# Kernel tuning notes

Hardware: AMD Instinct MI355X
Metric: run time of the kernel (lower is better)

The kernel has to match this reference:

```python
import jax, jax.numpy as jnp
import numpy as np

D_MODEL = 1024
NUM_HEADS = 16
D_HEAD = D_MODEL // NUM_HEADS
PATCH = 128


def setup_inputs() -> dict:
    key = jax.random.key(0)
    ks = jax.random.split(key, 10)
    B, T = 4, 8192
    x = jax.random.normal(ks[0], (B, T, D_MODEL), dtype=jnp.float32)
    coords = jax.random.uniform(ks[1], (B, T, 2), dtype=jnp.float32)
    s = 1.0 / np.sqrt(D_MODEL)
    Wq = jax.random.normal(ks[2], (D_MODEL, D_MODEL), dtype=jnp.float32) * s
    Wk = jax.random.normal(ks[3], (D_MODEL, D_MODEL), dtype=jnp.float32) * s
    Wv = jax.random.normal(ks[4], (D_MODEL, D_MODEL), dtype=jnp.float32) * s
    Wo = jax.random.normal(ks[5], (D_MODEL, D_MODEL), dtype=jnp.float32) * s
    bq = jnp.zeros((D_MODEL,), jnp.float32)
    bk = jnp.zeros((D_MODEL,), jnp.float32)
    bv = jnp.zeros((D_MODEL,), jnp.float32)
    bo = jnp.zeros((D_MODEL,), jnp.float32)
    return {"x": x, "coords": coords, "Wq": Wq, "bq": bq, "Wk": Wk, "bk": bk,
            "Wv": Wv, "bv": bv, "Wo": Wo, "bo": bo}


def _patched_attn(x, Wq, bq, Wk, bk, Wv, bv, Wo, bo):
    B, T, D = x.shape
    P = PATCH
    pad_len = (P - T % P) % P
    if pad_len > 0:
        x = jnp.pad(x, ((0, 0), (0, pad_len), (0, 0)))
    Tp = T + pad_len
    n = Tp // P
    xp = x.reshape(B * n, P, D)  # [N, P, D], independent patches
    def heads(y):  # [N, P, D] -> [N, H, P, dh]
        return y.reshape(B * n, P, NUM_HEADS, D_HEAD).transpose(0, 2, 1, 3)
    q = heads(xp @ Wq + bq)
    k = heads(xp @ Wk + bk)
    v = heads(xp @ Wv + bv)
    scores = jnp.einsum('bhtd,bhTd->bhtT', q, k) / jnp.sqrt(jnp.asarray(D_HEAD, x.dtype))
    w = jax.nn.softmax(scores, axis=-1)
    out = jnp.einsum('bhtT,bhTd->bhtd', w, v)
    out = out.transpose(0, 2, 1, 3).reshape(B * n, P, D)
    out = out @ Wo + bo
    out = out.reshape(B, Tp, D)
    if pad_len > 0:
        out = out[:, :T, :]
    return out


def reference(x, coords, Wq, bq, Wk, bk, Wv, bv, Wo, bo):
    # coords participates only in padding/reshape, not in the math
    return _patched_attn(x, Wq, bq, Wk, bk, Wv, bv, Wo, bo)
```

## Files before the change

### kernel.cpp

```cpp
#include <hip/hip_runtime.h>
#include <hip/hip_bf16.h>


#define DEV static __device__ __forceinline__

typedef __attribute__((ext_vector_type(8))) short short8;
typedef __attribute__((ext_vector_type(4))) float f32x4;

DEV unsigned short f2b(float f) {
  unsigned u = __builtin_bit_cast(unsigned, f);
  u += 0x7fffu + ((u >> 16) & 1u);
  return (unsigned short)(u >> 16);
}

DEV void load_lds16(const void* g, void* l) {
  __builtin_amdgcn_global_load_lds(
      (const __attribute__((address_space(1))) void*)g,
      (__attribute__((address_space(3))) void*)l, 16, 0, 0);
}

#define MFMA_BF16(a, b, c) __builtin_amdgcn_mfma_f32_16x16x32_bf16((a), (b), (c), 0, 0, 0)


__global__ void cvt_x_k(const float* __restrict__ x, unsigned short* __restrict__ xb, int n4) {
  int i = blockIdx.x * blockDim.x + threadIdx.x;
  int stride = gridDim.x * blockDim.x;
  for (; i < n4; i += stride) {
    float4 v = ((const float4*)x)[i];
    ushort4 o;
    o.x = f2b(v.x); o.y = f2b(v.y); o.z = f2b(v.z); o.w = f2b(v.w);
    ((ushort4*)xb)[i] = o;
  }
}

__global__ void twk4(const float* __restrict__ W0, const float* __restrict__ W1,
                     const float* __restrict__ W2, const float* __restrict__ W3,
                     unsigned short* __restrict__ Dqkv, unsigned short* __restrict__ Dot) {
  __shared__ unsigned short tile[64][65];
  const int w = blockIdx.x >> 8;
  const int t = blockIdx.x & 255;
  const float* W = (w == 0) ? W0 : (w == 1) ? W1 : (w == 2) ? W2 : W3;
  unsigned short* Wt = (w == 3) ? Dot : Dqkv + (size_t)w * 1024 * 1024;
  int k0 = (t >> 4) << 6;
  int n0 = (t & 15) << 6;
  int tx = threadIdx.x & 63;
  int ty = threadIdx.x >> 6;
#pragma unroll
  for (int i = 0; i < 16; ++i) {
    int r = (i << 2) + ty;
    tile[r][tx] = f2b(W[(size_t)(k0 + r) * 1024 + n0 + tx]);
  }
  __syncthreads();
#pragma unroll
  for (int i = 0; i < 16; ++i) {
    int n = (i << 2) + ty;
    Wt[(size_t)(n0 + n) * 1024 + k0 + tx] = tile[tx][n];
  }
}

__global__ void fuse_bias_k(const float* __restrict__ bq, const float* __restrict__ bk,
                            const float* __restrict__ bv, float* __restrict__ bqkv) {
  int i = blockIdx.x * 256 + threadIdx.x;
  if (i < 1024) bqkv[i] = bq[i];
  else if (i < 2048) bqkv[i] = bk[i - 1024];
  else if (i < 3072) bqkv[i] = bv[i - 2048];
}


template <bool OUT_F32>
__global__ __launch_bounds__(512, 2)
void gemm256(const unsigned short* __restrict__ A,
             const unsigned short* __restrict__ Bt,
             const float* __restrict__ bias,
             void* __restrict__ Cv, int M, int N, int K) {
  __shared__ __align__(16) unsigned short sh[65536];

  int nwg = gridDim.x, bid = blockIdx.x, wg = bid;
  if ((nwg & 7) == 0) {
    int cpx = nwg >> 3;
    wg = (bid & 7) * cpx + (bid >> 3);
  }
  const int nbn = N >> 8;
  const int bm = wg / nbn, bn = wg - bm * nbn;

  const int tid = threadIdx.x, lane = tid & 63, w = tid >> 6;
  const int wm = w >> 2, wn = w & 3;
  const int fr = lane & 15, g = lane >> 4;

  const int lr = lane >> 3;
  const int lb = ((lane & 7) << 4) ^ (lr << 4);
  const unsigned short* gsrc = (w < 4)
      ? A  + (size_t)(bm * 256 + w * 64 + lr) * K + (lb >> 1)
      : Bt + (size_t)(bn * 256 + (w - 4) * 64 + lr) * K + (lb >> 1);
  const int ldsw = w * 8192;

  const int koff0 = (g * 16) ^ ((fr & 7) << 4);
  const int koff1 = koff0 ^ 64;

  f32x4 acc[8][4] = {};
  const int NT = K >> 6;

  {
    char* l0 = (char*)sh + ldsw;
#pragma unroll
    for (int c = 0; c < 8; ++c)
      load_lds16(gsrc + (size_t)c * 8 * K, l0 + c * 1024);
  }

  for (int t = 0; t < NT; ++t) {
    if (t + 1 < NT) {
      const unsigned short* sN = gsrc + (size_t)(t + 1) * 64;
      char* lN = (char*)sh + ((t + 1) & 1) * 65536 + ldsw;
#pragma unroll
      for (int c = 0; c < 8; ++c)
        load_lds16(sN + (size_t)c * 8 * K, lN + c * 1024);
      asm volatile("s_waitcnt vmcnt(8)" ::: "memory");
    } else {
      asm volatile("s_waitcnt vmcnt(0)" ::: "memory");
    }
    __builtin_amdgcn_sched_barrier(0);
    __builtin_amdgcn_s_barrier();

    const char* bufp = (const char*)sh + (t & 1) * 65536;
    const char* ap0 = bufp + (wm * 128 + fr) * 128;
    const char* bp0 = bufp + 32768 + (wn * 64 + fr) * 128;

#pragma unroll
    for (int q = 0; q < 4; ++q) {
      const int mh = q >> 1, nh = q & 1;
      short8 af[4][2], bf[2][2];
      const char* ap = ap0 + mh * 64 * 128;
      const char* bp = bp0 + nh * 32 * 128;
#pragma unroll
      for (int ii = 0; ii < 4; ++ii) {
        af[ii][0] = *(const short8*)(ap + ii * 2048 + koff0);
        af[ii][1] = *(const short8*)(ap + ii * 2048 + koff1);
      }
#pragma unroll
      for (int jj = 0; jj < 2; ++jj) {
        bf[jj][0] = *(const short8*)(bp + jj * 2048 + koff0);
        bf[jj][1] = *(const short8*)(bp + jj * 2048 + koff1);
      }
      __builtin_amdgcn_s_barrier();
      asm volatile("s_waitcnt lgkmcnt(0)" ::: "memory");
      __builtin_amdgcn_sched_barrier(0);
      __builtin_amdgcn_s_setprio(1);
#pragma unroll
      for (int s = 0; s < 2; ++s)
#pragma unroll
        for (int ii = 0; ii < 4; ++ii)
#pragma unroll
          for (int jj = 0; jj < 2; ++jj)
            acc[mh * 4 + ii][nh * 2 + jj] =
                MFMA_BF16(af[ii][s], bf[jj][s], acc[mh * 4 + ii][nh * 2 + jj]);
      __builtin_amdgcn_s_setprio(0);
      __builtin_amdgcn_s_barrier();
    }
  }

  const int grow0 = bm * 256 + wm * 128 + g * 4;
  const int gcol0 = bn * 256 + wn * 64 + fr;
#pragma unroll
  for (int j = 0; j < 4; ++j) {
    const int gc = gcol0 + j * 16;
    const float bv_ = bias[gc];
#pragma unroll
    for (int i = 0; i < 8; ++i) {
      const int gr = grow0 + i * 16;
#pragma unroll
      for (int r = 0; r < 4; ++r) {
        float v = acc[i][j][r] + bv_;
        if (OUT_F32) ((float*)Cv)[(size_t)(gr + r) * N + gc] = v;
        else ((unsigned short*)Cv)[(size_t)(gr + r) * N + gc] = f2b(v);
      }
    }
  }
}


__global__ __launch_bounds__(256)
void attn_k(const unsigned short* __restrict__ qkv, unsigned short* __restrict__ out) {
  const int bh = blockIdx.x;
  const int p = bh >> 4, h = bh & 15;
  const int tid = threadIdx.x, lane = tid & 63, wv = tid >> 6;
  const int fr = lane & 15, fks = (lane >> 4) << 3;

  __shared__ __align__(16) unsigned short vt[64][136];
  __shared__ __align__(16) unsigned short pls[4][32][136];

  const size_t rowbase = (size_t)p * 128 * 3072;

  {
    const unsigned short* vsrc = qkv + rowbase + 2048 + (size_t)h * 64;
#pragma unroll
    for (int it = 0; it < 8; ++it) {
      int idx = tid + it * 256;
      int t = idx >> 4;
      int d4 = (idx & 15) << 2;
      ushort4 vv = *(const ushort4*)(vsrc + (size_t)t * 3072 + d4);
      vt[d4 + 0][t] = vv.x; vt[d4 + 1][t] = vv.y;
      vt[d4 + 2][t] = vv.z; vt[d4 + 3][t] = vv.w;
    }
  }

  short8 qf[2][2];
  {
    const unsigned short* qsrc = qkv + rowbase + (size_t)(wv * 32) * 3072 + h * 64;
#pragma unroll
    for (int mf = 0; mf < 2; ++mf)
#pragma unroll
      for (int kc = 0; kc < 2; ++kc)
        qf[mf][kc] = *(const short8*)(qsrc + (size_t)(mf * 16 + fr) * 3072 + kc * 32 + fks);
  }

  f32x4 s[2][8] = {};
  {
    const unsigned short* ksrc = qkv + rowbase + 1024 + (size_t)h * 64;
#pragma unroll
    for (int kc = 0; kc < 2; ++kc)
#pragma unroll
      for (int nf = 0; nf < 8; ++nf) {
        short8 kf = *(const short8*)(ksrc + (size_t)(nf * 16 + fr) * 3072 + kc * 32 + fks);
        s[0][nf] = MFMA_BF16(qf[0][kc], kf, s[0][nf]);
        s[1][nf] = MFMA_BF16(qf[1][kc], kf, s[1][nf]);
      }
  }
  __syncthreads();

  const float c0 = 0.125f * 1.44269504088896f;
  float sm[2][4];
#pragma unroll
  for (int mf = 0; mf < 2; ++mf)
#pragma unroll
    for (int r = 0; r < 4; ++r) {
      float m = s[mf][0][r];
#pragma unroll
      for (int nf = 1; nf < 8; ++nf) m = fmaxf(m, s[mf][nf][r]);
      m = fmaxf(m, __shfl_xor(m, 1));
      m = fmaxf(m, __shfl_xor(m, 2));
      m = fmaxf(m, __shfl_xor(m, 4));
      m = fmaxf(m, __shfl_xor(m, 8));
      float su = 0.f;
#pragma unroll
      for (int nf = 0; nf < 8; ++nf) {
        float e = exp2f((s[mf][nf][r] - m) * c0);
        s[mf][nf][r] = e;
        su += e;
      }
      su += __shfl_xor(su, 1);
      su += __shfl_xor(su, 2);
      su += __shfl_xor(su, 4);
      su += __shfl_xor(su, 8);
      sm[mf][r] = su;
    }

#pragma unroll
  for (int mf = 0; mf < 2; ++mf)
#pragma unroll
    for (int nf = 0; nf < 8; ++nf)
#pragma unroll
      for (int r = 0; r < 4; ++r)
        pls[wv][mf * 16 + ((lane >> 4) << 2) + r][nf * 16 + fr] = f2b(s[mf][nf][r]);

  f32x4 o[2][4] = {};
#pragma unroll
  for (int kc = 0; kc < 4; ++kc) {
    short8 pf0 = *(const short8*)&pls[wv][fr][kc * 32 + fks];
    short8 pf1 = *(const short8*)&pls[wv][16 + fr][kc * 32 + fks];
#pragma unroll
    for (int nf = 0; nf < 4; ++nf) {
      short8 vf = *(const short8*)&vt[nf * 16 + fr][kc * 32 + fks];
      o[0][nf] = MFMA_BF16(pf0, vf, o[0][nf]);
      o[1][nf] = MFMA_BF16(pf1, vf, o[1][nf]);
    }
  }

  unsigned short* obase = out + (size_t)(p * 128 + wv * 32) * 1024 + h * 64;
#pragma unroll
  for (int mf = 0; mf < 2; ++mf)
#pragma unroll
    for (int nf = 0; nf < 4; ++nf)
#pragma unroll
      for (int r = 0; r < 4; ++r) {
        int row = mf * 16 + ((lane >> 4) << 2) + r;
        float val = o[mf][nf][r] / sm[mf][r];
        obase[(size_t)row * 1024 + nf * 16 + fr] = f2b(val);
      }
}


extern "C" void kernel_launch(void* const* d_in, const int* in_sizes, int n_in,
                              void* d_out, int out_size, void* d_ws, size_t ws_size,
                              hipStream_t stream) {
  const float* x  = (const float*)d_in[0];
  const float* Wq = (const float*)d_in[2];
  const float* bq = (const float*)d_in[3];
  const float* Wk = (const float*)d_in[4];
  const float* bk = (const float*)d_in[5];
  const float* Wv = (const float*)d_in[6];
  const float* bv = (const float*)d_in[7];
  const float* Wo = (const float*)d_in[8];
  const float* bo = (const float*)d_in[9];

  char* ws = (char*)d_ws;
  unsigned short* xb   = (unsigned short*)(ws);
  unsigned short* wqkv = (unsigned short*)(ws + 67108864);
  unsigned short* wot  = (unsigned short*)(ws + 73400320);
  float*          bqkv = (float*)(ws + 75497472);
  unsigned short* qkv  = (unsigned short*)(ws + 75509760);

  cvt_x_k<<<2048, 256, 0, stream>>>(x, xb, (32768 * 1024) / 4);
  twk4<<<1024, 256, 0, stream>>>(Wq, Wk, Wv, Wo, wqkv, wot);
  fuse_bias_k<<<12, 256, 0, stream>>>(bq, bk, bv, bqkv);

  gemm256<false><<<1536, 512, 0, stream>>>(xb, wqkv, bqkv, qkv, 32768, 3072, 1024);
  attn_k<<<4096, 256, 0, stream>>>(qkv, xb);
  gemm256<true><<<512, 512, 0, stream>>>(xb, wot, bo, d_out, 32768, 1024, 1024);
}
```

Baseline: 718.7 us.

## Software-pipeline LDS fragment loads across GEMM quadrants with register double buffering

Restructures the GEMM main loop so LDS fragment reads for the next quadrant, and for the next K-tile, are issued while the MFMAs of the current quadrant run. It uses separate a0/a1/b0/b1 register sets and reorders the quadrants so A and B fragments get reused. This is meant to hide LDS latency that the old code exposed before each quadrant by waiting on lgkmcnt(0). The cost is higher register pressure and more complicated barrier and waitcnt logic, which could lower occupancy or add stalls. The epilogue loop order is also changed so that the bias loads are hoisted.

```diff
diff --git a/kernel.cpp b/kernel.cpp
--- a/kernel.cpp
+++ b/kernel.cpp
@@ -20,6 +20,8 @@
 }
 
 #define MFMA_BF16(a, b, c) __builtin_amdgcn_mfma_f32_16x16x32_bf16((a), (b), (c), 0, 0, 0)
+#define SB0() __builtin_amdgcn_sched_barrier(0)
+#define BAR() __builtin_amdgcn_s_barrier()
 
 
 __global__ void cvt_x_k(const float* __restrict__ x, unsigned short* __restrict__ xb, int n4) {
@@ -100,78 +102,138 @@
   f32x4 acc[8][4] = {};
   const int NT = K >> 6;
 
+  short8 a0[4][2], a1[4][2], b0[2][2], b1[2][2];
+
   {
     char* l0 = (char*)sh + ldsw;
 #pragma unroll
     for (int c = 0; c < 8; ++c)
       load_lds16(gsrc + (size_t)c * 8 * K, l0 + c * 1024);
+    asm volatile("s_waitcnt vmcnt(0)" ::: "memory");
+    BAR();
+    const char* ap = (const char*)sh + (wm * 128 + fr) * 128;
+    const char* bp = (const char*)sh + 32768 + (wn * 64 + fr) * 128;
+#pragma unroll
+    for (int ii = 0; ii < 4; ++ii) {
+      a0[ii][0] = *(const short8*)(ap + ii * 2048 + koff0);
+      a0[ii][1] = *(const short8*)(ap + ii * 2048 + koff1);
+    }
+#pragma unroll
+    for (int jj = 0; jj < 2; ++jj) {
+      b0[jj][0] = *(const short8*)(bp + jj * 2048 + koff0);
+      b0[jj][1] = *(const short8*)(bp + jj * 2048 + koff1);
+    }
   }
 
   for (int t = 0; t < NT; ++t) {
+    const char* bufc = (const char*)sh + (t & 1) * 65536;
+    const char* bufn = (const char*)sh + ((t + 1) & 1) * 65536;
+    const char* apc = bufc + (wm * 128 + fr) * 128;
+    const char* bpc = bufc + 32768 + (wn * 64 + fr) * 128;
+
     if (t + 1 < NT) {
       const unsigned short* sN = gsrc + (size_t)(t + 1) * 64;
       char* lN = (char*)sh + ((t + 1) & 1) * 65536 + ldsw;
 #pragma unroll
       for (int c = 0; c < 8; ++c)
         load_lds16(sN + (size_t)c * 8 * K, lN + c * 1024);
-      asm volatile("s_waitcnt vmcnt(8)" ::: "memory");
-    } else {
-      asm volatile("s_waitcnt vmcnt(0)" ::: "memory");
-    }
-    __builtin_amdgcn_sched_barrier(0);
-    __builtin_amdgcn_s_barrier();
-
-    const char* bufp = (const char*)sh + (t & 1) * 65536;
-    const char* ap0 = bufp + (wm * 128 + fr) * 128;
-    const char* bp0 = bufp + 32768 + (wn * 64 + fr) * 128;
-
-#pragma unroll
-    for (int q = 0; q < 4; ++q) {
-      const int mh = q >> 1, nh = q & 1;
-      short8 af[4][2], bf[2][2];
-      const char* ap = ap0 + mh * 64 * 128;
-      const char* bp = bp0 + nh * 32 * 128;
+    }
+#pragma unroll
+    for (int jj = 0; jj < 2; ++jj) {
+      b1[jj][0] = *(const short8*)(bpc + 32 * 128 + jj * 2048 + koff0);
+      b1[jj][1] = *(const short8*)(bpc + 32 * 128 + jj * 2048 + koff1);
+    }
+    BAR();
+    asm volatile("s_waitcnt lgkmcnt(4)" ::: "memory");
+    SB0();
+    __builtin_amdgcn_s_setprio(1);
+#pragma unroll
+    for (int s = 0; s < 2; ++s)
+#pragma unroll
+      for (int ii = 0; ii < 4; ++ii)
+#pragma unroll
+        for (int jj = 0; jj < 2; ++jj)
+          acc[ii][jj] = MFMA_BF16(a0[ii][s], b0[jj][s], acc[ii][jj]);
+    __builtin_amdgcn_s_setprio(0);
+    BAR();
+
+#pragma unroll
+    for (int ii = 0; ii < 4; ++ii) {
+      a1[ii][0] = *(const short8*)(apc + 64 * 128 + ii * 2048 + koff0);
+      a1[ii][1] = *(const short8*)(apc + 64 * 128 + ii * 2048 + koff1);
+    }
+    BAR();
+    asm volatile("s_waitcnt lgkmcnt(8)" ::: "memory");
+    SB0();
+    __builtin_amdgcn_s_setprio(1);
+#pragma unroll
+    for (int s = 0; s < 2; ++s)
+#pragma unroll
+      for (int ii = 0; ii < 4; ++ii)
+#pragma unroll
+        for (int jj = 0; jj < 2; ++jj)
+          acc[ii][2 + jj] = MFMA_BF16(a0[ii][s], b1[jj][s], acc[ii][2 + jj]);
+    __builtin_amdgcn_s_setprio(0);
+    BAR();
+
+    asm volatile("s_waitcnt vmcnt(0)" ::: "memory");
+    BAR();
+    asm volatile("s_waitcnt lgkmcnt(0)" ::: "memory");
+    SB0();
+    __builtin_amdgcn_s_setprio(1);
+#pragma unroll
+    for (int s = 0; s < 2; ++s)
+#pragma unroll
+      for (int ii = 0; ii < 4; ++ii)
+#pragma unroll
+        for (int jj = 0; jj < 2; ++jj)
+          acc[4 + ii][2 + jj] = MFMA_BF16(a1[ii][s], b1[jj][s], acc[4 + ii][2 + jj]);
+    __builtin_amdgcn_s_setprio(0);
+    BAR();
+
+    __builtin_amdgcn_s_setprio(1);
+#pragma unroll
+    for (int s = 0; s < 2; ++s)
+#pragma unroll
+      for (int ii = 0; ii < 4; ++ii)
+#pragma unroll
+        for (int jj = 0; jj < 2; ++jj)
+          acc[4 + ii][jj] = MFMA_BF16(a1[ii][s], b0[jj][s], acc[4 + ii][jj]);
+    __builtin_amdgcn_s_setprio(0);
+    SB0();
+    if (t + 1 < NT) {
+      const char* apn = bufn + (wm * 128 + fr) * 128;
+      const char* bpn = bufn + 32768 + (wn * 64 + fr) * 128;
 #pragma unroll
       for (int ii = 0; ii < 4; ++ii) {
-        af[ii][0] = *(const short8*)(ap + ii * 2048 + koff0);
-        af[ii][1] = *(const short8*)(ap + ii * 2048 + koff1);
+        a0[ii][0] = *(const short8*)(apn + ii * 2048 + koff0);
+        a0[ii][1] = *(const short8*)(apn + ii * 2048 + koff1);
       }
 #pragma unroll
       for (int jj = 0; jj < 2; ++jj) {
-        bf[jj][0] = *(const short8*)(bp + jj * 2048 + koff0);
-        bf[jj][1] = *(const short8*)(bp + jj * 2048 + koff1);
-      }
-      __builtin_amdgcn_s_barrier();
-      asm volatile("s_waitcnt lgkmcnt(0)" ::: "memory");
-      __builtin_amdgcn_sched_barrier(0);
-      __builtin_amdgcn_s_setprio(1);
-#pragma unroll
-      for (int s = 0; s < 2; ++s)
-#pragma unroll
-        for (int ii = 0; ii < 4; ++ii)
-#pragma unroll
-          for (int jj = 0; jj < 2; ++jj)
-            acc[mh * 4 + ii][nh * 2 + jj] =
-                MFMA_BF16(af[ii][s], bf[jj][s], acc[mh * 4 + ii][nh * 2 + jj]);
-      __builtin_amdgcn_s_setprio(0);
-      __builtin_amdgcn_s_barrier();
-    }
+        b0[jj][0] = *(const short8*)(bpn + jj * 2048 + koff0);
+        b0[jj][1] = *(const short8*)(bpn + jj * 2048 + koff1);
+      }
+    }
+    SB0();
+    BAR();
   }
 
   const int grow0 = bm * 256 + wm * 128 + g * 4;
   const int gcol0 = bn * 256 + wn * 64 + fr;
-#pragma unroll
-  for (int j = 0; j < 4; ++j) {
-    const int gc = gcol0 + j * 16;
-    const float bv_ = bias[gc];
-#pragma unroll
-    for (int i = 0; i < 8; ++i) {
-      const int gr = grow0 + i * 16;
-#pragma unroll
-      for (int r = 0; r < 4; ++r) {
-        float v = acc[i][j][r] + bv_;
-        if (OUT_F32) ((float*)Cv)[(size_t)(gr + r) * N + gc] = v;
-        else ((unsigned short*)Cv)[(size_t)(gr + r) * N + gc] = f2b(v);
+  float bv_[4];
+#pragma unroll
+  for (int j = 0; j < 4; ++j) bv_[j] = bias[gcol0 + j * 16];
+#pragma unroll
+  for (int i = 0; i < 8; ++i) {
+    const int gr = grow0 + i * 16;
+#pragma unroll
+    for (int r = 0; r < 4; ++r) {
+#pragma unroll
+      for (int j = 0; j < 4; ++j) {
+        float v = acc[i][j][r] + bv_[j];
+        if (OUT_F32) ((float*)Cv)[(size_t)(gr + r) * N + gcol0 + j * 16] = v;
+        else ((unsigned short*)Cv)[(size_t)(gr + r) * N + gcol0 + j * 16] = f2b(v);
       }
     }
   }
```

New measurement: 641.7 us. 10.7% less time.
